# Kernel tuning notes

Hardware: AMD Instinct MI355X
Metric: run time of the kernel (lower is better)

Reference implementation:

```python
import jax, jax.numpy as jnp
import numpy as np
from jax.ops import segment_sum, segment_max

N = 100000   # nodes
E = 1600000  # edges
B = 256      # graphs
H = 128      # hidden_channels
F_IN = 4     # input_size
EPS = 1e-5


def _graph_norm(x, w, b, ms, batch):
    # PyG GraphNorm: out = w * (x - ms*mean_g) / sqrt(var_g + eps) + b
    cnt = jnp.maximum(segment_sum(jnp.ones((x.shape[0],), x.dtype), batch, num_segments=B), 1.0)
    mean = segment_sum(x, batch, num_segments=B) / cnt[:, None]
    out = x - mean[batch] * ms
    var = segment_sum(out * out, batch, num_segments=B) / cnt[:, None]
    return w * out / jnp.sqrt(var + EPS)[batch] + b


def _gcn(x, W, b, src, dst):
    # GCNConv with self-loops and symmetric normalization (src/dst already include self-loops)
    h = x @ W                                              # [N, H]
    deg = segment_sum(jnp.ones_like(src, dtype=h.dtype), dst, num_segments=N)
    dinv = jax.lax.rsqrt(jnp.maximum(deg, 1.0))
    norm = dinv[src] * dinv[dst]                           # [E+N]
    return segment_sum(norm[:, None] * h[src], dst, num_segments=N) + b


def _seg_softmax(gate, batch):
    gmax = segment_max(gate, batch, num_segments=B)
    e = jnp.exp(gate - gmax[batch])
    den = segment_sum(e, batch, num_segments=B)
    return e / den[batch]


def setup_inputs() -> dict:
    key = jax.random.key(0)
    ks = jax.random.split(key, 16)
    x = jax.random.normal(ks[0], (N, F_IN), jnp.float32)
    edge_index = jax.random.randint(ks[1], (2, E), 0, N, dtype=jnp.int64)
    batch = jnp.sort(jax.random.randint(ks[2], (N,), 0, B, dtype=jnp.int64))
    r = lambda k, shp, fan: jax.random.normal(k, shp, jnp.float32) / np.sqrt(fan)
    inp = {
        "x": x, "edge_index": edge_index, "batch": batch,
        "W1": r(ks[3], (F_IN, H), F_IN), "b1": jnp.zeros((H,), jnp.float32),
        "W2": r(ks[4], (H, H), H), "b2": jnp.zeros((H,), jnp.float32),
        "W3": r(ks[5], (H, H), H), "b3": jnp.zeros((H,), jnp.float32),
        "gn0_w": jnp.ones((F_IN,), jnp.float32), "gn0_b": jnp.zeros((F_IN,), jnp.float32), "gn0_ms": jnp.ones((F_IN,), jnp.float32),
        "gn1_w": jnp.ones((H,), jnp.float32), "gn1_b": jnp.zeros((H,), jnp.float32), "gn1_ms": jnp.ones((H,), jnp.float32),
        "gn2_w": jnp.ones((H,), jnp.float32), "gn2_b": jnp.zeros((H,), jnp.float32), "gn2_ms": jnp.ones((H,), jnp.float32),
        "gn3_w": jnp.ones((H,), jnp.float32), "gn3_b": jnp.zeros((H,), jnp.float32), "gn3_ms": jnp.ones((H,), jnp.float32),
        "g1": r(ks[6], (H, H), H), "gb1": jnp.zeros((H,), jnp.float32),
        "g2": r(ks[7], (H, H), H), "gb2": jnp.zeros((H,), jnp.float32),
        "g3": r(ks[8], (H, 1), H), "gb3": jnp.zeros((1,), jnp.float32),
        "l1": r(ks[9], (H, H), H), "lb1": jnp.zeros((H,), jnp.float32),
        "l2": r(ks[10], (H, H), H), "lb2": jnp.zeros((H,), jnp.float32),
        "l3": r(ks[11], (H, 1), H), "lb3": jnp.zeros((1,), jnp.float32),
    }
    return inp


def reference(x, edge_index, batch, W1, b1, W2, b2, W3, b3,
              gn0_w, gn0_b, gn0_ms, gn1_w, gn1_b, gn1_ms,
              gn2_w, gn2_b, gn2_ms, gn3_w, gn3_b, gn3_ms,
              g1, gb1, g2, gb2, g3, gb3,
              l1, lb1, l2, lb2, l3, lb3):
    loop = jnp.arange(N, dtype=edge_index.dtype)
    src = jnp.concatenate([edge_index[0], loop])
    dst = jnp.concatenate([edge_index[1], loop])

    h = _graph_norm(x, gn0_w, gn0_b, gn0_ms, batch)
    h = _gcn(h, W1, b1, src, dst)
    h = jax.nn.relu(_graph_norm(h, gn1_w, gn1_b, gn1_ms, batch))
    h = _gcn(h, W2, b2, src, dst)
    h = jax.nn.relu(_graph_norm(h, gn2_w, gn2_b, gn2_ms, batch))
    h = _gcn(h, W3, b3, src, dst)
    h = _graph_norm(h, gn3_w, gn3_b, gn3_ms, batch)

    # GlobalAttention: gate_nn -> scalar gate per node, segment softmax, weighted sum
    g = jax.nn.relu(h @ g1 + gb1)
    g = jax.nn.relu(g @ g2 + gb2)
    gate = g @ g3 + gb3                                   # [N, 1]
    attn = _seg_softmax(gate, batch)                      # [N, 1]
    pooled = segment_sum(attn * h, batch, num_segments=B) # [B, H]

    o = jax.nn.relu(pooled @ l1 + lb1)
    o = jax.nn.relu(o @ l2 + lb2)
    return o @ l3 + lb3                                   # [B, 1]
```

## Files before the change

### kernel.cpp

```cpp
#include <hip/hip_runtime.h>
#include <hip/hip_bf16.h>

#define NN 100000
#define NE 1600000
#define NB 256
#define HD 128
#define EPS 1e-5f
#define NBUK 1563
#define SLOTB 1536
#define EPB 2048
#define NCHK 8

typedef __attribute__((ext_vector_type(8))) short bf16x8v;
typedef __attribute__((ext_vector_type(4))) float f32x4v;

__device__ __forceinline__ float rd_dyn(const void* p, int i, int fflag) {
    if (fflag) {
        unsigned short u = ((const unsigned short*)p)[i];
        return __uint_as_float(((unsigned)u) << 16);
    }
    return ((const float*)p)[i];
}

__device__ __forceinline__ int rd_idx(const int* p, int k, int iflag) {
    return iflag ? p[k] : p[2 * k];
}

__device__ __forceinline__ unsigned short f2bf(float v) {
    __hip_bfloat16 b = __float2bfloat16(v);
    return *(unsigned short*)&b;
}

__device__ __forceinline__ float bflo(unsigned u) { return __uint_as_float(u << 16); }
__device__ __forceinline__ float bfhi(unsigned u) { return __uint_as_float(u & 0xFFFF0000u); }
__device__ __forceinline__ unsigned packbf(float a, float b) {
    return (unsigned)f2bf(a) | ((unsigned)f2bf(b) << 16);
}

__global__ void k_mark7(unsigned short* __restrict__ out, int n) {
    int i = blockIdx.x * blockDim.x + threadIdx.x;
    if (i < n) out[i] = 0x40E0;
}

__global__ void k_detect(const int* __restrict__ batch, const unsigned* __restrict__ w,
                         int* __restrict__ flags, int n) {
    int i = blockIdx.x * blockDim.x + threadIdx.x;
    if (i == 0 && w[0] == 0x3F803F80u) atomicOr(&flags[1], 1);
    if (i < n && (i & 1) && batch[i] != 0) atomicOr(&flags[0], 1);
}

struct CvtArgs {
    const void* p[30];
    int n[30];
    int off[30];
    const void* wp[4];
};
__global__ void k_prep(CvtArgs a, float* __restrict__ out,
                       unsigned short* __restrict__ WT,
                       const int* __restrict__ flagsp,
                       const int* __restrict__ batch,
                       int* __restrict__ start, int* __restrict__ batch32,
                       int* __restrict__ bcur) {
    int j = blockIdx.y;
    int i = blockIdx.x * blockDim.x + threadIdx.x;
    if (j < 30) {
        if (i >= a.n[j]) return;
        out[a.off[j] + i] = rd_dyn(a.p[j], i, flagsp[1]);
    } else if (j < 34) {
        int mat = j - 30;
        if (i >= 16384) return;
        int nidx = i >> 7, k = i & 127;
        WT[mat * 16384 + nidx * 128 + k] = f2bf(rd_dyn(a.wp[mat], k * 128 + nidx, flagsp[1]));
    } else {
        if (i >= NN) return;
        if (i < NBUK) bcur[i] = i * SLOTB;
        int ifl = flagsp[0];
        int b = rd_idx(batch, i, ifl); b = b < 0 ? 0 : (b > NB - 1 ? NB - 1 : b);
        batch32[i] = b;
        int bp;
        if (i == 0) bp = -1;
        else { bp = rd_idx(batch, i - 1, ifl); bp = bp < 0 ? 0 : (bp > NB - 1 ? NB - 1 : bp); }
        for (int g = bp + 1; g <= b; ++g) start[g] = i;
        if (i == NN - 1) { for (int g = b + 1; g <= NB; ++g) start[g] = NN; }
    }
}

__global__ __launch_bounds__(256) void k_bfill(const int* __restrict__ ei,
                                               const int* __restrict__ iflagp,
                                               int* __restrict__ bcur,
                                               unsigned* __restrict__ bkte, int e) {
    __shared__ int lh[NBUK];
    __shared__ int lbase[NBUK];
    int ifl = *iflagp;
    for (int b = threadIdx.x; b < NBUK; b += 256) lh[b] = 0;
    __syncthreads();
    int s0 = blockIdx.x * EPB;
    int s1 = s0 + EPB; if (s1 > e) s1 = e;
    for (int i = s0 + threadIdx.x; i < s1; i += 256) {
        int d = rd_idx(ei, NE + i, ifl);
        int s = rd_idx(ei, i, ifl);
        if ((unsigned)d < (unsigned)NN && (unsigned)s < (unsigned)NN)
            atomicAdd(&lh[d >> 6], 1);
    }
    __syncthreads();
    for (int b = threadIdx.x; b < NBUK; b += 256) {
        int c = lh[b];
        if (c) { lbase[b] = atomicAdd(&bcur[b], c); lh[b] = 0; }
    }
    __syncthreads();
    for (int i = s0 + threadIdx.x; i < s1; i += 256) {
        int d = rd_idx(ei, NE + i, ifl);
        int s = rd_idx(ei, i, ifl);
        if ((unsigned)d < (unsigned)NN && (unsigned)s < (unsigned)NN) {
            int b = d >> 6;
            int li = atomicAdd(&lh[b], 1);
            bkte[lbase[b] + li] = ((unsigned)s << 6) | (unsigned)(d & 63);
        }
    }
}

__global__ __launch_bounds__(256) void k_csrfin_gn4(const unsigned* __restrict__ bkte,
                                                    const int* __restrict__ bcur,
                                                    int* __restrict__ rowptr,
                                                    int* __restrict__ cnt,
                                                    float* __restrict__ dinv,
                                                    int* __restrict__ esrc,
                                                    const void* __restrict__ x,
                                                    const float* __restrict__ w,
                                                    const float* __restrict__ bb,
                                                    const float* __restrict__ ms,
                                                    const int* __restrict__ start,
                                                    const int* __restrict__ fflagp,
                                                    float* __restrict__ out) {
    int t = threadIdx.x;
    if (blockIdx.x < NBUK) {
        __shared__ int lc[64];
        __shared__ int lcur[64];
        int b = blockIdx.x;
        int base = b * 64;
        if (t < 64) lc[t] = 0;
        __syncthreads();
        int r0 = b * SLOTB, r1 = bcur[b];
        for (int j = r0 + t; j < r1; j += 256)
            atomicAdd(&lc[(int)(bkte[j] & 63u)], 1);
        __syncthreads();
        if (t < 64) {
            int v = lc[t];
            int inc = v;
#pragma unroll
            for (int off = 1; off < 64; off <<= 1) {
                int nv = __shfl_up(inc, off, 64);
                if (t >= off) inc += nv;
            }
            int ex = r0 + inc - v;
            lcur[t] = ex;
            int node = base + t;
            if (node < NN) {
                rowptr[node] = ex;
                cnt[node] = v;
                dinv[node] = rsqrtf((float)(v + 1));
            }
        }
        __syncthreads();
        for (int j = r0 + t; j < r1; j += 256) {
            unsigned p = bkte[j];
            int slot = atomicAdd(&lcur[p & 63u], 1);
            esrc[slot] = (int)(p >> 6);
        }
        return;
    }
    __shared__ float4 rs[256], rq[256];
    int g = blockIdx.x - NBUK;
    int s0 = start[g], s1 = start[g + 1];
    if (s1 <= s0) return;
    int ff = *fflagp;
    float cntf = (float)(s1 - s0);
    float sx = 0.f, sy = 0.f, sz = 0.f, sw = 0.f;
    float qx = 0.f, qy = 0.f, qz = 0.f, qw = 0.f;
    for (int n = s0 + t; n < s1; n += 256) {
        float4 v;
        if (ff) {
            uint2 u = ((const uint2*)x)[n];
            v.x = bflo(u.x); v.y = bfhi(u.x); v.z = bflo(u.y); v.w = bfhi(u.y);
        } else {
            v = ((const float4*)x)[n];
        }
        sx += v.x; sy += v.y; sz += v.z; sw += v.w;
        qx = fmaf(v.x, v.x, qx); qy = fmaf(v.y, v.y, qy);
        qz = fmaf(v.z, v.z, qz); qw = fmaf(v.w, v.w, qw);
    }
    rs[t] = make_float4(sx, sy, sz, sw);
    rq[t] = make_float4(qx, qy, qz, qw);
    __syncthreads();
    for (int off = 128; off; off >>= 1) {
        if (t < off) {
            rs[t].x += rs[t + off].x; rs[t].y += rs[t + off].y;
            rs[t].z += rs[t + off].z; rs[t].w += rs[t + off].w;
            rq[t].x += rq[t + off].x; rq[t].y += rq[t + off].y;
            rq[t].z += rq[t + off].z; rq[t].w += rq[t + off].w;
        }
        __syncthreads();
    }
    float4 S = rs[0], Q = rq[0];
    float4 wv = ((const float4*)w)[0];
    float4 bv = ((const float4*)bb)[0];
    float4 mv = ((const float4*)ms)[0];
    float4 mean = make_float4(S.x / cntf, S.y / cntf, S.z / cntf, S.w / cntf);
    float4 sub = make_float4(mean.x * mv.x, mean.y * mv.y, mean.z * mv.z, mean.w * mv.w);
    float4 scale;
    scale.x = wv.x * rsqrtf(Q.x / cntf - 2.f * sub.x * mean.x + sub.x * sub.x + EPS);
    scale.y = wv.y * rsqrtf(Q.y / cntf - 2.f * sub.y * mean.y + sub.y * sub.y + EPS);
    scale.z = wv.z * rsqrtf(Q.z / cntf - 2.f * sub.z * mean.z + sub.z * sub.z + EPS);
    scale.w = wv.w * rsqrtf(Q.w / cntf - 2.f * sub.w * mean.w + sub.w * sub.w + EPS);
    float4* op = (float4*)out;
    for (int n = s0 + t; n < s1; n += 256) {
        float4 v;
        if (ff) {
            uint2 u = ((const uint2*)x)[n];
            v.x = bflo(u.x); v.y = bfhi(u.x); v.z = bflo(u.y); v.w = bfhi(u.y);
        } else {
            v = ((const float4*)x)[n];
        }
        float4 o;
        o.x = scale.x * (v.x - sub.x) + bv.x;
        o.y = scale.y * (v.y - sub.y) + bv.y;
        o.z = scale.z * (v.z - sub.z) + bv.z;
        o.w = scale.w * (v.w - sub.w) + bv.w;
        op[n] = o;
    }
}

__global__ __launch_bounds__(256) void k_gnstats1(const unsigned* __restrict__ Xu,
                                                  const float* __restrict__ w,
                                                  const float* __restrict__ ms,
                                                  const int* __restrict__ start,
                                                  float* __restrict__ SUB,
                                                  float* __restrict__ SCALE) {
    int g = blockIdx.x, seg = blockIdx.y;
    int s0 = start[g], s1 = start[g + 1];
    if (s1 <= s0) return;
    int t = threadIdx.x;
    int wrd = t & 15;
    int p = t >> 4;
    int wbase = seg * 16 + wrd;
    __shared__ float rs0[256], rs1[256], rq0[256], rq1[256];
    float sa = 0.f, sb = 0.f, qa = 0.f, qb = 0.f;
    for (int n = s0 + p; n < s1; n += 16) {
        unsigned u = Xu[(size_t)n * 64 + wbase];
        float lo = bflo(u), hi = bfhi(u);
        sa += lo; qa = fmaf(lo, lo, qa);
        sb += hi; qb = fmaf(hi, hi, qb);
    }
    rs0[t] = sa; rs1[t] = sb; rq0[t] = qa; rq1[t] = qb;
    __syncthreads();
    for (int off = 128; off >= 16; off >>= 1) {
        if (t < off) {
            rs0[t] += rs0[t + off]; rs1[t] += rs1[t + off];
            rq0[t] += rq0[t + off]; rq1[t] += rq1[t + off];
        }
        __syncthreads();
    }
    if (t < 16) {
        float cnt = (float)(s1 - s0);
        int c0 = 2 * (seg * 16 + t), c1 = c0 + 1;
        float mean0 = rs0[t] / cnt, mean1 = rs1[t] / cnt;
        float sub0 = mean0 * ms[c0], sub1 = mean1 * ms[c1];
        float var0 = rq0[t] / cnt - 2.f * sub0 * mean0 + sub0 * sub0;
        float var1 = rq1[t] / cnt - 2.f * sub1 * mean1 + sub1 * sub1;
        SUB[g * 128 + c0] = sub0; SUB[g * 128 + c1] = sub1;
        SCALE[g * 128 + c0] = w[c0] * rsqrtf(var0 + EPS);
        SCALE[g * 128 + c1] = w[c1] * rsqrtf(var1 + EPS);
    }
}

__global__ __launch_bounds__(256) void k_gather4gemm(const int* __restrict__ rowptr,
                                                     const int* __restrict__ cnt,
                                                     const int* __restrict__ esrc,
                                                     const float* __restrict__ dinv,
                                                     const float* __restrict__ h0,
                                                     const float* __restrict__ W1,
                                                     const float* __restrict__ b1,
                                                     unsigned* __restrict__ Xu) {
    __shared__ float w1s[512];
    __shared__ float b1s[128];
    int tid = threadIdx.x;
    w1s[tid] = W1[tid];
    w1s[256 + tid] = W1[256 + tid];
    if (tid < 128) b1s[tid] = b1[tid];
    __syncthreads();
    int node = blockIdx.x * 4 + (tid >> 6);
    int lane = tid & 63;
    if (node >= NN) return;
    int ch = lane & 3;
    int r0 = rowptr[node], r1 = r0 + cnt[node];
    float acc = 0.f;
    for (int j = r0 + (lane >> 2); j < r1; j += 16) {
        int s = esrc[j];
        acc = fmaf(dinv[s], h0[s * 4 + ch], acc);
    }
#pragma unroll
    for (int mask = 4; mask <= 32; mask <<= 1)
        acc += __shfl_xor(acc, mask, 64);
    float dd = dinv[node];
    float z = dd * acc + dd * dd * h0[node * 4 + ch];
    float za = __shfl(z, 0, 64), zb = __shfl(z, 1, 64);
    float zc = __shfl(z, 2, 64), zd = __shfl(z, 3, 64);
    int c0 = 2 * lane, c1 = 2 * lane + 1;
    float v0 = za * w1s[c0] + zb * w1s[128 + c0] + zc * w1s[256 + c0] + zd * w1s[384 + c0] + b1s[c0];
    float v1 = za * w1s[c1] + zb * w1s[128 + c1] + zc * w1s[256 + c1] + zd * w1s[384 + c1] + b1s[c1];
    Xu[node * 64 + lane] = packbf(v0, v1);
}

__global__ __launch_bounds__(256) void k_gemm_mfma_bf(const unsigned* __restrict__ Xu,
                                                      const int* __restrict__ batch32,
                                                      const float* __restrict__ SUB,
                                                      const float* __restrict__ SCALE,
                                                      const float* __restrict__ gnb,
                                                      int relu,
                                                      const unsigned short* __restrict__ WT,
                                                      const float* __restrict__ dinv,
                                                      unsigned short* __restrict__ out) {
    __shared__ unsigned short xs[16][136];
    int base = blockIdx.x * 16;
    int tid = threadIdx.x;
    for (int idx = tid; idx < 1024; idx += 256) {
        int r = idx >> 6, cp = idx & 63;
        int g = batch32[base + r];
        unsigned u = Xu[(base + r) * 64 + cp];
        float2 sub = ((const float2*)(SUB + g * 128))[cp];
        float2 sc  = ((const float2*)(SCALE + g * 128))[cp];
        float2 gb  = ((const float2*)gnb)[cp];
        float va = (bflo(u) - sub.x) * sc.x + gb.x;
        float vb = (bfhi(u) - sub.y) * sc.y + gb.y;
        if (relu) { va = fmaxf(va, 0.f); vb = fmaxf(vb, 0.f); }
        xs[r][2 * cp] = f2bf(va);
        xs[r][2 * cp + 1] = f2bf(vb);
    }
    __syncthreads();
    int wave = tid >> 6, lane = tid & 63;
    int m = lane & 15, quad = lane >> 4;
    f32x4v acc0 = {0.f, 0.f, 0.f, 0.f}, acc1 = {0.f, 0.f, 0.f, 0.f};
    int c0 = wave * 32 + m, c1 = c0 + 16;
#pragma unroll
    for (int kk = 0; kk < 4; ++kk) {
        int ko = kk * 32 + quad * 8;
        bf16x8v a  = *(const bf16x8v*)&xs[m][ko];
        bf16x8v b0 = *(const bf16x8v*)&WT[c0 * 128 + ko];
        bf16x8v b1 = *(const bf16x8v*)&WT[c1 * 128 + ko];
        acc0 = __builtin_amdgcn_mfma_f32_16x16x32_bf16(a, b0, acc0, 0, 0, 0);
        acc1 = __builtin_amdgcn_mfma_f32_16x16x32_bf16(a, b1, acc1, 0, 0, 0);
    }
#pragma unroll
    for (int reg = 0; reg < 4; ++reg) {
        int row = base + quad * 4 + reg;
        float dv = dinv[row];
        out[row * 128 + c0] = f2bf(dv * acc0[reg]);
        out[row * 128 + c1] = f2bf(dv * acc1[reg]);
    }
}

#define ACC4(u) do { \
    a0 += bflo((u).x); a1 += bfhi((u).x); \
    a2 += bflo((u).y); a3 += bfhi((u).y); \
    a4 += bflo((u).z); a5 += bfhi((u).z); \
    a6 += bflo((u).w); a7 += bfhi((u).w); } while (0)

__global__ __launch_bounds__(256) void k_gather_bf(const int* __restrict__ rowptr,
                                                   const int* __restrict__ cnt,
                                                   const int* __restrict__ esrc,
                                                   const float* __restrict__ dinv,
                                                   const unsigned* __restrict__ h,
                                                   const float* __restrict__ bias,
                                                   unsigned* __restrict__ Xu) {
    int node = blockIdx.x * 4 + (threadIdx.x >> 6);
    int lane = threadIdx.x & 63;
    if (node >= NN) return;
    int q = lane >> 4, s = lane & 15;
    int r0 = rowptr[node], r1 = r0 + cnt[node];
    const uint4* hp = (const uint4*)h;
    float a0 = 0.f, a1 = 0.f, a2 = 0.f, a3 = 0.f;
    float a4 = 0.f, a5 = 0.f, a6 = 0.f, a7 = 0.f;
    int j = r0 + q;
    for (; j + 12 < r1; j += 16) {
        int e0 = esrc[j], e1 = esrc[j + 4], e2 = esrc[j + 8], e3 = esrc[j + 12];
        uint4 u0 = hp[e0 * 16 + s];
        uint4 u1 = hp[e1 * 16 + s];
        uint4 u2 = hp[e2 * 16 + s];
        uint4 u3 = hp[e3 * 16 + s];
        ACC4(u0); ACC4(u1); ACC4(u2); ACC4(u3);
    }
    for (; j + 4 < r1; j += 8) {
        int e0 = esrc[j], e1 = esrc[j + 4];
        uint4 u0 = hp[e0 * 16 + s];
        uint4 u1 = hp[e1 * 16 + s];
        ACC4(u0); ACC4(u1);
    }
    for (; j < r1; j += 4) {
        int e0 = esrc[j];
        uint4 u0 = hp[e0 * 16 + s];
        ACC4(u0);
    }
    a0 += __shfl_xor(a0, 16, 64); a0 += __shfl_xor(a0, 32, 64);
    a1 += __shfl_xor(a1, 16, 64); a1 += __shfl_xor(a1, 32, 64);
    a2 += __shfl_xor(a2, 16, 64); a2 += __shfl_xor(a2, 32, 64);
    a3 += __shfl_xor(a3, 16, 64); a3 += __shfl_xor(a3, 32, 64);
    a4 += __shfl_xor(a4, 16, 64); a4 += __shfl_xor(a4, 32, 64);
    a5 += __shfl_xor(a5, 16, 64); a5 += __shfl_xor(a5, 32, 64);
    a6 += __shfl_xor(a6, 16, 64); a6 += __shfl_xor(a6, 32, 64);
    a7 += __shfl_xor(a7, 16, 64); a7 += __shfl_xor(a7, 32, 64);
    int cp = 4 * s + q;
    float ax = q == 0 ? a0 : q == 1 ? a2 : q == 2 ? a4 : a6;
    float ay = q == 0 ? a1 : q == 1 ? a3 : q == 2 ? a5 : a7;
    float dd = dinv[node];
    unsigned us = h[node * 64 + cp];
    float2 bb = ((const float2*)bias)[cp];
    float ox = dd * (ax + bflo(us)) + bb.x;
    float oy = dd * (ay + bfhi(us)) + bb.y;
    Xu[node * 64 + cp] = packbf(ox, oy);
}

__global__ __launch_bounds__(256) void k_gate_fused(const unsigned* __restrict__ Xu,
                                                    const int* __restrict__ batch32,
                                                    const float* __restrict__ SUB,
                                                    const float* __restrict__ SCALE,
                                                    const float* __restrict__ gnb,
                                                    const unsigned short* __restrict__ GT1,
                                                    const float* __restrict__ gb1,
                                                    const unsigned short* __restrict__ GT2,
                                                    const float* __restrict__ gb2,
                                                    const float* __restrict__ g3,
                                                    const float* __restrict__ gb3,
                                                    float* __restrict__ gate) {
    __shared__ unsigned short xs[16][136];
    __shared__ unsigned short t1[16][136];
    __shared__ float redw[64];
    int base = blockIdx.x * 16;
    int tid = threadIdx.x;
    for (int idx = tid; idx < 1024; idx += 256) {
        int r = idx >> 6, cp = idx & 63;
        int g = batch32[base + r];
        unsigned u = Xu[(base + r) * 64 + cp];
        float2 sub = ((const float2*)(SUB + g * 128))[cp];
        float2 sc  = ((const float2*)(SCALE + g * 128))[cp];
        float2 gb  = ((const float2*)gnb)[cp];
        xs[r][2 * cp] = f2bf((bflo(u) - sub.x) * sc.x + gb.x);
        xs[r][2 * cp + 1] = f2bf((bfhi(u) - sub.y) * sc.y + gb.y);
    }
    __syncthreads();
    int wave = tid >> 6, lane = tid & 63;
    int m = lane & 15, quad = lane >> 4;
    int c0 = wave * 32 + m, c1 = c0 + 16;
    f32x4v acc0 = {0.f, 0.f, 0.f, 0.f}, acc1 = {0.f, 0.f, 0.f, 0.f};
#pragma unroll
    for (int kk = 0; kk < 4; ++kk) {
        int ko = kk * 32 + quad * 8;
        bf16x8v a  = *(const bf16x8v*)&xs[m][ko];
        bf16x8v b0 = *(const bf16x8v*)&GT1[c0 * 128 + ko];
        bf16x8v b1 = *(const bf16x8v*)&GT1[c1 * 128 + ko];
        acc0 = __builtin_amdgcn_mfma_f32_16x16x32_bf16(a, b0, acc0, 0, 0, 0);
        acc1 = __builtin_amdgcn_mfma_f32_16x16x32_bf16(a, b1, acc1, 0, 0, 0);
    }
    float bj0 = gb1[c0], bj1 = gb1[c1];
#pragma unroll
    for (int reg = 0; reg < 4; ++reg) {
        int row = quad * 4 + reg;
        t1[row][c0] = f2bf(fmaxf(acc0[reg] + bj0, 0.f));
        t1[row][c1] = f2bf(fmaxf(acc1[reg] + bj1, 0.f));
    }
    __syncthreads();
    f32x4v d0 = {0.f, 0.f, 0.f, 0.f}, d1 = {0.f, 0.f, 0.f, 0.f};
#pragma unroll
    for (int kk = 0; kk < 4; ++kk) {
        int ko = kk * 32 + quad * 8;
        bf16x8v a  = *(const bf16x8v*)&t1[m][ko];
        bf16x8v b0 = *(const bf16x8v*)&GT2[c0 * 128 + ko];
        bf16x8v b1 = *(const bf16x8v*)&GT2[c1 * 128 + ko];
        d0 = __builtin_amdgcn_mfma_f32_16x16x32_bf16(a, b0, d0, 0, 0, 0);
        d1 = __builtin_amdgcn_mfma_f32_16x16x32_bf16(a, b1, d1, 0, 0, 0);
    }
    float g30 = g3[c0], g31 = g3[c1];
    float bk0 = gb2[c0], bk1 = gb2[c1];
    float contrib[4];
#pragma unroll
    for (int reg = 0; reg < 4; ++reg) {
        float v0 = fmaxf(d0[reg] + bk0, 0.f);
        float v1 = fmaxf(d1[reg] + bk1, 0.f);
        contrib[reg] = v0 * g30 + v1 * g31;
    }
#pragma unroll
    for (int mask = 1; mask <= 8; mask <<= 1) {
#pragma unroll
        for (int reg = 0; reg < 4; ++reg)
            contrib[reg] += __shfl_xor(contrib[reg], mask, 64);
    }
    if (m == 0) {
#pragma unroll
        for (int reg = 0; reg < 4; ++reg)
            redw[wave * 16 + quad * 4 + reg] = contrib[reg];
    }
    __syncthreads();
    if (tid < 16) {
        float s = redw[tid] + redw[16 + tid] + redw[32 + tid] + redw[48 + tid];
        gate[base + tid] = s + gb3[0];
    }
}

__global__ __launch_bounds__(256) void k_smpool(const unsigned* __restrict__ Xu,
                                                const float* __restrict__ SUB,
                                                const float* __restrict__ SCALE,
                                                const float* __restrict__ gnb,
                                                const float* __restrict__ gate,
                                                const int* __restrict__ start,
                                                float* __restrict__ PP) {
    int g = blockIdx.x, kk = blockIdx.y;
    int s0 = start[g], s1 = start[g + 1];
    int t = threadIdx.x;
    __shared__ float red[256];
    __shared__ float r0s[256], r1s[256];
    if (s1 <= s0) {
        if (t < 64) {
            int bidx = (g * NCHK + kk) * 128;
            ((float2*)(PP + bidx))[t] = make_float2(0.f, 0.f);
        }
        return;
    }
    float m = -1e30f;
    for (int i = s0 + t; i < s1; i += 256) m = fmaxf(m, gate[i]);
    red[t] = m; __syncthreads();
    for (int off = 128; off; off >>= 1) { if (t < off) red[t] = fmaxf(red[t], red[t + off]); __syncthreads(); }
    m = red[0]; __syncthreads();
    float sden = 0.f;
    for (int i = s0 + t; i < s1; i += 256) sden += expf(gate[i] - m);
    red[t] = sden; __syncthreads();
    for (int off = 128; off; off >>= 1) { if (t < off) red[t] += red[t + off]; __syncthreads(); }
    float invden = 1.f / red[0];
    int len = (s1 - s0 + NCHK - 1) / NCHK;
    int c0 = s0 + kk * len, c1 = c0 + len; if (c1 > s1) c1 = s1;
    int cp = t & 63, p = t >> 6;
    float2 sub = ((const float2*)(SUB + g * 128))[cp];
    float2 sc  = ((const float2*)(SCALE + g * 128))[cp];
    float2 gb  = ((const float2*)gnb)[cp];
    float sa = 0.f, sb = 0.f;
    for (int n = c0 + p; n < c1; n += 4) {
        float a = expf(gate[n] - m) * invden;
        unsigned u = Xu[n * 64 + cp];
        sa += a * ((bflo(u) - sub.x) * sc.x + gb.x);
        sb += a * ((bfhi(u) - sub.y) * sc.y + gb.y);
    }
    r0s[t] = sa; r1s[t] = sb; __syncthreads();
    if (p == 0) {
        int bidx = (g * NCHK + kk) * 128;
        float2 o;
        o.x = r0s[cp] + r0s[64 + cp] + r0s[128 + cp] + r0s[192 + cp];
        o.y = r1s[cp] + r1s[64 + cp] + r1s[128 + cp] + r1s[192 + cp];
        ((float2*)(PP + bidx))[cp] = o;
    }
}

__global__ __launch_bounds__(128) void k_head(const float* __restrict__ PP,
                                              const float* __restrict__ l1, const float* __restrict__ lb1,
                                              const float* __restrict__ l2, const float* __restrict__ lb2,
                                              const float* __restrict__ l3, const float* __restrict__ lb3,
                                              const int* __restrict__ fflagp,
                                              void* __restrict__ out) {
    int g = blockIdx.x, t = threadIdx.x;
    __shared__ float p[128], o[128], red[128];
    float s = 0.f;
#pragma unroll
    for (int k = 0; k < NCHK; ++k) s += PP[(g * NCHK + k) * 128 + t];
    p[t] = s; __syncthreads();
    float a = 0.f;
    for (int k = 0; k < 128; ++k) a += p[k] * l1[k * 128 + t];
    a = fmaxf(a + lb1[t], 0.f);
    o[t] = a; __syncthreads();
    float b = 0.f;
    for (int k = 0; k < 128; ++k) b += o[k] * l2[k * 128 + t];
    b = fmaxf(b + lb2[t], 0.f);
    red[t] = b * l3[t]; __syncthreads();
    for (int off = 64; off; off >>= 1) { if (t < off) red[t] += red[t + off]; __syncthreads(); }
    if (t == 0) {
        float r = red[0] + lb3[0];
        if (*fflagp) ((__hip_bfloat16*)out)[g] = __float2bfloat16(r);
        else ((float*)out)[g] = r;
    }
}

extern "C" void kernel_launch(void* const* d_in, const int* in_sizes, int n_in,
                              void* d_out, int out_size, void* d_ws, size_t ws_size,
                              hipStream_t stream) {
    const void* x = d_in[0];
    const int* ei_raw = (const int*)d_in[1];
    const int* batch_raw = (const int*)d_in[2];
    (void)n_in; (void)out_size;

    char* ws = (char*)d_ws;
    size_t off = 0;
    auto alloc = [&](size_t bytes) -> void* {
        void* p = ws + off;
        off += (bytes + 255) & ~(size_t)255;
        return p;
    };
    unsigned* Xu  = (unsigned*)alloc((size_t)NN * HD * 2);
    float* Y      = (float*)alloc((size_t)NN * HD * 4);
    float* h0     = (float*)alloc((size_t)NN * 4 * 4);
    float* dinv   = (float*)alloc((size_t)NN * 4);
    float* gate   = (float*)alloc((size_t)NN * 4);
    int*   start  = (int*)alloc((size_t)(NB + 1) * 4);
    int*   batch32= (int*)alloc((size_t)NN * 4);
    float* P      = (float*)alloc((size_t)131072 * 4);
    unsigned short* WT = (unsigned short*)alloc((size_t)4 * 16384 * 2);
    float* SUB    = (float*)alloc((size_t)NB * HD * 4);
    float* SCALE  = (float*)alloc((size_t)NB * HD * 4);
    float* PP     = (float*)alloc((size_t)NB * NCHK * 128 * 4);
    int*   flags  = (int*)alloc(256);
    int*   rowptr = (int*)alloc((size_t)NN * 4);
    int*   cnt    = (int*)alloc((size_t)NN * 4);
    int*   esrc   = (int*)alloc((size_t)NBUK * SLOTB * 4);
    int*   bcur   = (int*)alloc((size_t)NBUK * 4);
    unsigned* bkte = (unsigned*)(Y + (size_t)NN * HD / 2);

    if (ws_size < off) {
        k_mark7<<<1, 256, 0, stream>>>((unsigned short*)d_out, NB);
        return;
    }

    int* iflag = flags;
    int* fflag = flags + 1;
    hipMemsetAsync(flags, 0, 8, stream);
    k_detect<<<(NN + 255) / 256, 256, 0, stream>>>(batch_raw, (const unsigned*)d_in[12], flags, NN);

    CvtArgs ca;
    float* fp[33];
    {
        int poff = 0;
        for (int i = 3; i < 33; ++i) {
            int n = in_sizes[i];
            ca.p[i - 3] = d_in[i];
            ca.n[i - 3] = n;
            ca.off[i - 3] = poff;
            fp[i] = P + poff;
            poff += n;
        }
        ca.wp[0] = d_in[5];
        ca.wp[1] = d_in[7];
        ca.wp[2] = d_in[21];
        ca.wp[3] = d_in[23];
    }
    {
        dim3 grid((NN + 255) / 256, 35);
        k_prep<<<grid, 256, 0, stream>>>(ca, P, WT, flags, batch_raw, start, batch32, bcur);
    }
    const float *W1 = fp[3], *b1 = fp[4], *b2 = fp[6], *b3 = fp[8];
    const float *gn0w = fp[9],  *gn0b = fp[10], *gn0m = fp[11];
    const float *gn1w = fp[12], *gn1m = fp[14], *gn1b = fp[13];
    const float *gn2w = fp[15], *gn2b = fp[16], *gn2m = fp[17];
    const float *gn3w = fp[18], *gn3b = fp[19], *gn3m = fp[20];
    const float *gb1 = fp[22], *gb2 = fp[24], *g3 = fp[25], *gb3 = fp[26];
    const float *l1 = fp[27], *lb1 = fp[28], *l2 = fp[29], *lb2 = fp[30], *l3 = fp[31], *lb3 = fp[32];

    const unsigned short* WT2 = WT;
    const unsigned short* WT3 = WT + 16384;
    const unsigned short* GT1 = WT + 2 * 16384;
    const unsigned short* GT2 = WT + 3 * 16384;

    int ebg = (NE + EPB - 1) / EPB;
    k_bfill<<<ebg, 256, 0, stream>>>(ei_raw, iflag, bcur, bkte, NE);
    k_csrfin_gn4<<<NBUK + NB, 256, 0, stream>>>(bkte, bcur, rowptr, cnt, dinv, esrc,
                                                x, gn0w, gn0b, gn0m, start, fflag, h0);

    k_gather4gemm<<<(NN + 3) / 4, 256, 0, stream>>>(rowptr, cnt, esrc, dinv, h0, W1, b1, Xu);

    unsigned short* Yb = (unsigned short*)Y;
    dim3 sgrid(NB, 4);
    dim3 pgrid(NB, NCHK);

    k_gnstats1<<<sgrid, 256, 0, stream>>>(Xu, gn1w, gn1m, start, SUB, SCALE);
    k_gemm_mfma_bf<<<NN / 16, 256, 0, stream>>>(Xu, batch32, SUB, SCALE, gn1b, 1, WT2, dinv, Yb);
    k_gather_bf<<<(NN + 3) / 4, 256, 0, stream>>>(rowptr, cnt, esrc, dinv, (const unsigned*)Yb, b2, Xu);

    k_gnstats1<<<sgrid, 256, 0, stream>>>(Xu, gn2w, gn2m, start, SUB, SCALE);
    k_gemm_mfma_bf<<<NN / 16, 256, 0, stream>>>(Xu, batch32, SUB, SCALE, gn2b, 1, WT3, dinv, Yb);
    k_gather_bf<<<(NN + 3) / 4, 256, 0, stream>>>(rowptr, cnt, esrc, dinv, (const unsigned*)Yb, b3, Xu);

    k_gnstats1<<<sgrid, 256, 0, stream>>>(Xu, gn3w, gn3m, start, SUB, SCALE);
    k_gate_fused<<<NN / 16, 256, 0, stream>>>(Xu, batch32, SUB, SCALE, gn3b,
                                              GT1, gb1, GT2, gb2, g3, gb3, gate);
    k_smpool<<<pgrid, 256, 0, stream>>>(Xu, SUB, SCALE, gn3b, gate, start, PP);
    k_head<<<NB, 128, 0, stream>>>(PP, l1, lb1, l2, lb2, l3, lb3, fflag, d_out);
}
```

Baseline: 542.8 us.

## Use direct global atomics for edge bucketing and widen bf16 loads to 4 elements

The edge-bucketing kernel drops its two-pass shared-memory histogram with per-block reservation and instead does one global atomicAdd per edge on the bucket cursor, in a grid-stride loop over 2048 blocks. Separately, the GraphNorm stats, GEMM prologue and attention pooling kernels now load uint2 (four bf16) and float4 parameters per thread instead of unsigned/float2, which halves the load instruction count. The global-atomic bucketing removes shared-memory passes and syncs but adds 1.6M contended global atomics, and edge order within buckets becomes nondeterministic.

```diff
diff --git a/kernel.cpp b/kernel.cpp
--- a/kernel.cpp
+++ b/kernel.cpp
@@ -8,7 +8,6 @@
 #define EPS 1e-5f
 #define NBUK 1563
 #define SLOTB 1536
-#define EPB 2048
 #define NCHK 8
 
 typedef __attribute__((ext_vector_type(8))) short bf16x8v;
@@ -89,32 +88,15 @@
                                                const int* __restrict__ iflagp,
                                                int* __restrict__ bcur,
                                                unsigned* __restrict__ bkte, int e) {
-    __shared__ int lh[NBUK];
-    __shared__ int lbase[NBUK];
     int ifl = *iflagp;
-    for (int b = threadIdx.x; b < NBUK; b += 256) lh[b] = 0;
-    __syncthreads();
-    int s0 = blockIdx.x * EPB;
-    int s1 = s0 + EPB; if (s1 > e) s1 = e;
-    for (int i = s0 + threadIdx.x; i < s1; i += 256) {
-        int d = rd_idx(ei, NE + i, ifl);
-        int s = rd_idx(ei, i, ifl);
-        if ((unsigned)d < (unsigned)NN && (unsigned)s < (unsigned)NN)
-            atomicAdd(&lh[d >> 6], 1);
-    }
-    __syncthreads();
-    for (int b = threadIdx.x; b < NBUK; b += 256) {
-        int c = lh[b];
-        if (c) { lbase[b] = atomicAdd(&bcur[b], c); lh[b] = 0; }
-    }
-    __syncthreads();
-    for (int i = s0 + threadIdx.x; i < s1; i += 256) {
+    int i = blockIdx.x * 256 + threadIdx.x;
+    int stride = gridDim.x * 256;
+    for (; i < e; i += stride) {
         int d = rd_idx(ei, NE + i, ifl);
         int s = rd_idx(ei, i, ifl);
         if ((unsigned)d < (unsigned)NN && (unsigned)s < (unsigned)NN) {
-            int b = d >> 6;
-            int li = atomicAdd(&lh[b], 1);
-            bkte[lbase[b] + li] = ((unsigned)s << 6) | (unsigned)(d & 63);
+            int slot = atomicAdd(&bcur[d >> 6], 1);
+            bkte[slot] = ((unsigned)s << 6) | (unsigned)(d & 63);
         }
     }
 }
@@ -240,36 +222,45 @@
     int s0 = start[g], s1 = start[g + 1];
     if (s1 <= s0) return;
     int t = threadIdx.x;
-    int wrd = t & 15;
-    int p = t >> 4;
-    int wbase = seg * 16 + wrd;
-    __shared__ float rs0[256], rs1[256], rq0[256], rq1[256];
-    float sa = 0.f, sb = 0.f, qa = 0.f, qb = 0.f;
-    for (int n = s0 + p; n < s1; n += 16) {
-        unsigned u = Xu[(size_t)n * 64 + wbase];
-        float lo = bflo(u), hi = bfhi(u);
-        sa += lo; qa = fmaf(lo, lo, qa);
-        sb += hi; qb = fmaf(hi, hi, qb);
-    }
-    rs0[t] = sa; rs1[t] = sb; rq0[t] = qa; rq1[t] = qb;
-    __syncthreads();
-    for (int off = 128; off >= 16; off >>= 1) {
+    int u2i = t & 7;
+    int p = t >> 3;
+    __shared__ float4 rs[256], rq[256];
+    float s0a = 0.f, s1a = 0.f, s2a = 0.f, s3a = 0.f;
+    float q0a = 0.f, q1a = 0.f, q2a = 0.f, q3a = 0.f;
+    int idx2 = seg * 8 + u2i;
+    for (int n = s0 + p; n < s1; n += 32) {
+        uint2 v = ((const uint2*)(Xu + (size_t)n * 64))[idx2];
+        float a = bflo(v.x), b = bfhi(v.x), c = bflo(v.y), d = bfhi(v.y);
+        s0a += a; q0a = fmaf(a, a, q0a);
+        s1a += b; q1a = fmaf(b, b, q1a);
+        s2a += c; q2a = fmaf(c, c, q2a);
+        s3a += d; q3a = fmaf(d, d, q3a);
+    }
+    rs[t] = make_float4(s0a, s1a, s2a, s3a);
+    rq[t] = make_float4(q0a, q1a, q2a, q3a);
+    __syncthreads();
+    for (int off = 128; off >= 8; off >>= 1) {
         if (t < off) {
-            rs0[t] += rs0[t + off]; rs1[t] += rs1[t + off];
-            rq0[t] += rq0[t + off]; rq1[t] += rq1[t + off];
+            rs[t].x += rs[t + off].x; rs[t].y += rs[t + off].y;
+            rs[t].z += rs[t + off].z; rs[t].w += rs[t + off].w;
+            rq[t].x += rq[t + off].x; rq[t].y += rq[t + off].y;
+            rq[t].z += rq[t + off].z; rq[t].w += rq[t + off].w;
         }
         __syncthreads();
     }
-    if (t < 16) {
+    if (t < 8) {
         float cnt = (float)(s1 - s0);
-        int c0 = 2 * (seg * 16 + t), c1 = c0 + 1;
-        float mean0 = rs0[t] / cnt, mean1 = rs1[t] / cnt;
-        float sub0 = mean0 * ms[c0], sub1 = mean1 * ms[c1];
-        float var0 = rq0[t] / cnt - 2.f * sub0 * mean0 + sub0 * sub0;
-        float var1 = rq1[t] / cnt - 2.f * sub1 * mean1 + sub1 * sub1;
-        SUB[g * 128 + c0] = sub0; SUB[g * 128 + c1] = sub1;
-        SCALE[g * 128 + c0] = w[c0] * rsqrtf(var0 + EPS);
-        SCALE[g * 128 + c1] = w[c1] * rsqrtf(var1 + EPS);
+        int c = seg * 32 + t * 4;
+        float S[4] = {rs[t].x, rs[t].y, rs[t].z, rs[t].w};
+        float Q[4] = {rq[t].x, rq[t].y, rq[t].z, rq[t].w};
+#pragma unroll
+        for (int k = 0; k < 4; ++k) {
+            float mean = S[k] / cnt;
+            float sub = mean * ms[c + k];
+            float var = Q[k] / cnt - 2.f * sub * mean + sub * sub;
+            SUB[g * 128 + c + k] = sub;
+            SCALE[g * 128 + c + k] = w[c + k] * rsqrtf(var + EPS);
+        }
     }
 }
 
@@ -323,18 +314,24 @@
     __shared__ unsigned short xs[16][136];
     int base = blockIdx.x * 16;
     int tid = threadIdx.x;
-    for (int idx = tid; idx < 1024; idx += 256) {
-        int r = idx >> 6, cp = idx & 63;
+#pragma unroll
+    for (int it = 0; it < 2; ++it) {
+        int idx = tid + it * 256;
+        int r = idx >> 5, cp2 = idx & 31;
         int g = batch32[base + r];
-        unsigned u = Xu[(base + r) * 64 + cp];
-        float2 sub = ((const float2*)(SUB + g * 128))[cp];
-        float2 sc  = ((const float2*)(SCALE + g * 128))[cp];
-        float2 gb  = ((const float2*)gnb)[cp];
-        float va = (bflo(u) - sub.x) * sc.x + gb.x;
-        float vb = (bfhi(u) - sub.y) * sc.y + gb.y;
-        if (relu) { va = fmaxf(va, 0.f); vb = fmaxf(vb, 0.f); }
-        xs[r][2 * cp] = f2bf(va);
-        xs[r][2 * cp + 1] = f2bf(vb);
+        uint2 u = ((const uint2*)(Xu + (size_t)(base + r) * 64))[cp2];
+        float4 sub = ((const float4*)(SUB + g * 128))[cp2];
+        float4 sc  = ((const float4*)(SCALE + g * 128))[cp2];
+        float4 gb  = ((const float4*)gnb)[cp2];
+        float va = (bflo(u.x) - sub.x) * sc.x + gb.x;
+        float vb = (bfhi(u.x) - sub.y) * sc.y + gb.y;
+        float vc = (bflo(u.y) - sub.z) * sc.z + gb.z;
+        float vd = (bfhi(u.y) - sub.w) * sc.w + gb.w;
+        if (relu) {
+            va = fmaxf(va, 0.f); vb = fmaxf(vb, 0.f);
+            vc = fmaxf(vc, 0.f); vd = fmaxf(vd, 0.f);
+        }
+        *(uint2*)&xs[r][4 * cp2] = make_uint2(packbf(va, vb), packbf(vc, vd));
     }
     __syncthreads();
     int wave = tid >> 6, lane = tid & 63;
@@ -436,15 +433,20 @@
     __shared__ float redw[64];
     int base = blockIdx.x * 16;
     int tid = threadIdx.x;
-    for (int idx = tid; idx < 1024; idx += 256) {
-        int r = idx >> 6, cp = idx & 63;
+#pragma unroll
+    for (int it = 0; it < 2; ++it) {
+        int idx = tid + it * 256;
+        int r = idx >> 5, cp2 = idx & 31;
         int g = batch32[base + r];
-        unsigned u = Xu[(base + r) * 64 + cp];
-        float2 sub = ((const float2*)(SUB + g * 128))[cp];
-        float2 sc  = ((const float2*)(SCALE + g * 128))[cp];
-        float2 gb  = ((const float2*)gnb)[cp];
-        xs[r][2 * cp] = f2bf((bflo(u) - sub.x) * sc.x + gb.x);
-        xs[r][2 * cp + 1] = f2bf((bfhi(u) - sub.y) * sc.y + gb.y);
+        uint2 u = ((const uint2*)(Xu + (size_t)(base + r) * 64))[cp2];
+        float4 sub = ((const float4*)(SUB + g * 128))[cp2];
+        float4 sc  = ((const float4*)(SCALE + g * 128))[cp2];
+        float4 gb  = ((const float4*)gnb)[cp2];
+        float va = (bflo(u.x) - sub.x) * sc.x + gb.x;
+        float vb = (bfhi(u.x) - sub.y) * sc.y + gb.y;
+        float vc = (bflo(u.y) - sub.z) * sc.z + gb.z;
+        float vd = (bfhi(u.y) - sub.w) * sc.w + gb.w;
+        *(uint2*)&xs[r][4 * cp2] = make_uint2(packbf(va, vb), packbf(vc, vd));
     }
     __syncthreads();
     int wave = tid >> 6, lane = tid & 63;
@@ -516,11 +518,11 @@
     int s0 = start[g], s1 = start[g + 1];
     int t = threadIdx.x;
     __shared__ float red[256];
-    __shared__ float r0s[256], r1s[256];
+    __shared__ float4 rs4[256];
     if (s1 <= s0) {
-        if (t < 64) {
+        if (t < 32) {
             int bidx = (g * NCHK + kk) * 128;
-            ((float2*)(PP + bidx))[t] = make_float2(0.f, 0.f);
+            ((float4*)(PP + bidx))[t] = make_float4(0.f, 0.f, 0.f, 0.f);
         }
         return;
     }
@@ -536,24 +538,31 @@
     float invden = 1.f / red[0];
     int len = (s1 - s0 + NCHK - 1) / NCHK;
     int c0 = s0 + kk * len, c1 = c0 + len; if (c1 > s1) c1 = s1;
-    int cp = t & 63, p = t >> 6;
-    float2 sub = ((const float2*)(SUB + g * 128))[cp];
-    float2 sc  = ((const float2*)(SCALE + g * 128))[cp];
-    float2 gb  = ((const float2*)gnb)[cp];
-    float sa = 0.f, sb = 0.f;
-    for (int n = c0 + p; n < c1; n += 4) {
+    int cp2 = t & 31, p = t >> 5;
+    float4 sub = ((const float4*)(SUB + g * 128))[cp2];
+    float4 sc  = ((const float4*)(SCALE + g * 128))[cp2];
+    float4 gb  = ((const float4*)gnb)[cp2];
+    float a0 = 0.f, a1 = 0.f, a2 = 0.f, a3 = 0.f;
+    for (int n = c0 + p; n < c1; n += 8) {
         float a = expf(gate[n] - m) * invden;
-        unsigned u = Xu[n * 64 + cp];
-        sa += a * ((bflo(u) - sub.x) * sc.x + gb.x);
-        sb += a * ((bfhi(u) - sub.y) * sc.y + gb.y);
-    }
-    r0s[t] = sa; r1s[t] = sb; __syncthreads();
-    if (p == 0) {
+        uint2 u = ((const uint2*)(Xu + (size_t)n * 64))[cp2];
+        a0 += a * ((bflo(u.x) - sub.x) * sc.x + gb.x);
+        a1 += a * ((bfhi(u.x) - sub.y) * sc.y + gb.y);
+        a2 += a * ((bflo(u.y) - sub.z) * sc.z + gb.z);
+        a3 += a * ((bfhi(u.y) - sub.w) * sc.w + gb.w);
+    }
+    rs4[t] = make_float4(a0, a1, a2, a3);
+    __syncthreads();
+    for (int off = 128; off >= 32; off >>= 1) {
+        if (t < off) {
+            rs4[t].x += rs4[t + off].x; rs4[t].y += rs4[t + off].y;
+            rs4[t].z += rs4[t + off].z; rs4[t].w += rs4[t + off].w;
+        }
+        __syncthreads();
+    }
+    if (t < 32) {
         int bidx = (g * NCHK + kk) * 128;
-        float2 o;
-        o.x = r0s[cp] + r0s[64 + cp] + r0s[128 + cp] + r0s[192 + cp];
-        o.y = r1s[cp] + r1s[64 + cp] + r1s[128 + cp] + r1s[192 + cp];
-        ((float2*)(PP + bidx))[cp] = o;
+        ((float4*)(PP + bidx))[t] = rs4[t];
     }
 }
 
@@ -663,8 +672,7 @@
     const unsigned short* GT1 = WT + 2 * 16384;
     const unsigned short* GT2 = WT + 3 * 16384;
 
-    int ebg = (NE + EPB - 1) / EPB;
-    k_bfill<<<ebg, 256, 0, stream>>>(ei_raw, iflag, bcur, bkte, NE);
+    k_bfill<<<2048, 256, 0, stream>>>(ei_raw, iflag, bcur, bkte, NE);
     k_csrfin_gn4<<<NBUK + NB, 256, 0, stream>>>(bkte, bcur, rowptr, cnt, dinv, esrc,
                                                 x, gn0w, gn0b, gn0m, start, fflag, h0);
 
```

Measured after the change: 713.4 us. 31.4% more time.
